# Kernel tuning notes

Hardware: AMD Instinct MI355X
Metric: run time of the kernel (lower is better)

## Reference

```python
import jax, jax.numpy as jnp
import numpy as np


def setup_inputs() -> dict:
    key = jax.random.key(0)
    k1, k2, k3 = jax.random.split(key, 3)
    B, C_in, H, W = 32, 128, 64, 64
    C_out, KH, KW = 256, 3, 3
    x = jax.random.normal(k1, (B, C_in, H, W), dtype=jnp.float32)
    # kaiming_normal fan_out scale ~ sqrt(2 / (C_out*KH*KW)); plain normal is fine for a numeric reference
    weight = jax.random.normal(k2, (C_out, C_in, KH, KW), dtype=jnp.float32) * (2.0 / (C_out * KH * KW)) ** 0.5
    fan_in = C_in * KH * KW
    bound = 1.0 / (fan_in ** 0.5)
    bias = jax.random.uniform(k3, (C_out,), dtype=jnp.float32, minval=-bound, maxval=bound)
    return {"x": x, "weight": weight, "bias": bias}


def reference(x, weight, bias):
    # Equivalent of unfold (im2col) + matmul + fold with stride=1, padding=1:
    # a standard 2D convolution in NCHW/OIHW layout.
    out = jax.lax.conv_general_dilated(
        x, weight,
        window_strides=(1, 1),
        padding=((1, 1), (1, 1)),
        dimension_numbers=("NCHW", "OIHW", "NCHW"),
    )
    return out + bias[None, :, None, None]
```

## Files before the change

### kernel.cpp

```cpp
#include <hip/hip_runtime.h>

typedef __attribute__((ext_vector_type(4))) int   v4i;
typedef __attribute__((ext_vector_type(8))) short s8;
typedef __attribute__((ext_vector_type(4))) float f32x4;
typedef __attribute__((ext_vector_type(16))) float f32x16;

#define GLB __attribute__((address_space(1)))
#define LDS_AS __attribute__((address_space(3)))

__device__ __forceinline__ unsigned short f2bf(float f) {
  unsigned u = __builtin_bit_cast(unsigned, f);
  return (unsigned short)((u + 0x7fffu + ((u >> 16) & 1u)) >> 16);
}

__global__ void wprep(const float* __restrict__ w, unsigned short* __restrict__ ww) {
  int o = blockIdx.x * 256 + threadIdx.x;
  int tap = o >> 15;
  int c   = (o >> 13) & 3;
  int cog = (o >> 10) & 7;
  int kk  = (o >> 9) & 1;
  int lh  = (o >> 8) & 1;
  int l31 = (o >> 3) & 31;
  int e   = o & 7;
  int co = cog * 32 + l31;
  int ci = c * 32 + kk * 16 + lh * 8 + e;
  ww[o] = f2bf(w[(co * 128 + ci) * 9 + tap]);
}

__global__ void xprep(const float* __restrict__ x, unsigned int* __restrict__ xw) {
  __shared__ float tile[128][65];
  int bid = blockIdx.x;
  int b = bid >> 6, h = bid & 63;
  int t = threadIdx.x;
  {
    int wcol = t & 63, cl = t >> 6;
    const float* src = x + ((size_t)(b * 128) * 64 + h) * 64 + wcol;
#pragma unroll
    for (int j = 0; j < 32; ++j) {
      int ci = j * 4 + cl;
      tile[ci][wcol] = src[(size_t)ci * 4096];
    }
  }
  unsigned int* dst = xw + (size_t)((b * 66 + h + 1) * 66) * 64;
  if (t < 128) {
    int col = (t >> 6) ? 65 : 0;
    dst[(size_t)col * 64 + (t & 63)] = 0u;
  }
  if (h == 0 || h == 63) {
    unsigned int* rb = xw + (size_t)(b * 66 + (h == 0 ? 0 : 65)) * 66 * 64;
    for (int j = t; j < 66 * 64; j += 256) rb[j] = 0u;
  }
  __syncthreads();
  {
    int ci2 = (t & 63) * 2, wl = t >> 6;
#pragma unroll
    for (int j = 0; j < 16; ++j) {
      int wcol = j * 4 + wl;
      unsigned p = (unsigned)f2bf(tile[ci2][wcol]) |
                   ((unsigned)f2bf(tile[ci2 + 1][wcol]) << 16);
      dst[(size_t)(wcol + 1) * 64 + (t & 63)] = p;
    }
  }
}

__global__ __launch_bounds__(256, 3) void conv_mfma(
    const unsigned short* __restrict__ xw, const unsigned short* __restrict__ ww,
    const float* __restrict__ bias, float* __restrict__ out) {
  __shared__ unsigned short Xl[204 * 128];
  const int tid = threadIdx.x;
  const int lane = tid & 63;
  const int l31 = lane & 31, lh = lane >> 5;
  const int mw = tid >> 6;
  int bid = blockIdx.x;
  bid = (bid & 7) * 256 + (bid >> 3);
  const int b = bid >> 6, h0 = bid & 63;

  {
    const char* xbase = (const char*)xw;
#pragma unroll
    for (int it = 0; it < 13; ++it) {
      int s = tid + it * 256;
      if (s < 3264) {
        int q = s >> 4, p = s & 15;
        int u = p ^ (q & 15);
        int rr = q / 68, cc = q - rr * 68;
        if (cc > 65) cc = 65;
        unsigned src = (unsigned)((b * 66 + h0 + rr) * 66 + cc) * 256u + (unsigned)u * 16u;
        __builtin_amdgcn_global_load_lds((const GLB unsigned int*)(xbase + src),
                                         (LDS_AS unsigned int*)&Xl[s * 8], 16, 0, 0);
      }
    }
  }

  f32x16 acc[2][2];
#pragma unroll
  for (int m = 0; m < 2; ++m)
#pragma unroll
    for (int n = 0; n < 2; ++n)
#pragma unroll
      for (int e = 0; e < 16; ++e) acc[m][n][e] = 0.f;

  v4i areg[3][4];
  const unsigned abyte = (unsigned)(mw * 4096 + lane * 16);

  #define ALOAD_ASM(slot, step)                                               \
    do {                                                                      \
      unsigned _wo = (unsigned)(step) * 16384u + abyte;                       \
      asm volatile("global_load_dwordx4 %0, %1, %2 offset:0"                  \
                   : "=v"(areg[slot][0]) : "v"(_wo), "s"(ww));                \
      asm volatile("global_load_dwordx4 %0, %1, %2 offset:1024"               \
                   : "=v"(areg[slot][1]) : "v"(_wo), "s"(ww));                \
      asm volatile("global_load_dwordx4 %0, %1, %2 offset:2048"               \
                   : "=v"(areg[slot][2]) : "v"(_wo), "s"(ww));                \
      asm volatile("global_load_dwordx4 %0, %1, %2 offset:3072"               \
                   : "=v"(areg[slot][3]) : "v"(_wo), "s"(ww));                \
    } while (0)

  const char* Xlb = (const char*)Xl;

  __syncthreads();

  ALOAD_ASM(0, 0);
  ALOAD_ASM(1, 1);

#pragma unroll
  for (int s = 0; s < 36; ++s) {
    if (s < 34) ALOAD_ASM((s + 2) % 3, s + 2);

    const int _tap = s >> 2, _c = s & 3;
    const int _kh = _tap / 3, _kw = _tap - _kh * 3;
    const int _qt0 = _kh * 68 + _kw + l31;
    const int _qt1 = _qt0 + 32;
    const int _b0 = _qt0 << 8, _b1 = _qt1 << 8;
    const int _x0 = (_qt0 & 15) ^ lh, _x1 = (_qt1 & 15) ^ lh;
    s8 b00 = *(const s8*)(Xlb + _b0 + (((_c * 4) ^ _x0) << 4));
    s8 b10 = *(const s8*)(Xlb + _b1 + (((_c * 4) ^ _x1) << 4));
    s8 b01 = *(const s8*)(Xlb + _b0 + (((_c * 4 + 2) ^ _x0) << 4));
    s8 b11 = *(const s8*)(Xlb + _b1 + (((_c * 4 + 2) ^ _x1) << 4));

    if (s < 34)      asm volatile("s_waitcnt vmcnt(8)" ::: "memory");
    else if (s == 34) asm volatile("s_waitcnt vmcnt(4)" ::: "memory");
    else              asm volatile("s_waitcnt vmcnt(0)" ::: "memory");
    __builtin_amdgcn_sched_barrier(0);

    const int cs = s % 3;
    __builtin_amdgcn_s_setprio(1);
    acc[0][0] = __builtin_amdgcn_mfma_f32_32x32x16_bf16(__builtin_bit_cast(s8, areg[cs][0]), b00, acc[0][0], 0, 0, 0);
    acc[1][0] = __builtin_amdgcn_mfma_f32_32x32x16_bf16(__builtin_bit_cast(s8, areg[cs][2]), b00, acc[1][0], 0, 0, 0);
    acc[0][1] = __builtin_amdgcn_mfma_f32_32x32x16_bf16(__builtin_bit_cast(s8, areg[cs][0]), b10, acc[0][1], 0, 0, 0);
    acc[1][1] = __builtin_amdgcn_mfma_f32_32x32x16_bf16(__builtin_bit_cast(s8, areg[cs][2]), b10, acc[1][1], 0, 0, 0);
    acc[0][0] = __builtin_amdgcn_mfma_f32_32x32x16_bf16(__builtin_bit_cast(s8, areg[cs][1]), b01, acc[0][0], 0, 0, 0);
    acc[1][0] = __builtin_amdgcn_mfma_f32_32x32x16_bf16(__builtin_bit_cast(s8, areg[cs][3]), b01, acc[1][0], 0, 0, 0);
    acc[0][1] = __builtin_amdgcn_mfma_f32_32x32x16_bf16(__builtin_bit_cast(s8, areg[cs][1]), b11, acc[0][1], 0, 0, 0);
    acc[1][1] = __builtin_amdgcn_mfma_f32_32x32x16_bf16(__builtin_bit_cast(s8, areg[cs][3]), b11, acc[1][1], 0, 0, 0);
    __builtin_amdgcn_s_setprio(0);
  }

#pragma unroll
  for (int m = 0; m < 2; ++m)
#pragma unroll
    for (int rq = 0; rq < 4; ++rq) {
      const int cob = mw * 64 + m * 32 + 8 * rq + 4 * lh;
      const f32x4 bi = *(const f32x4*)(bias + cob);
#pragma unroll
      for (int n = 0; n < 2; ++n) {
        const int wc = n * 32 + l31;
        size_t base = ((size_t)(b * 256 + cob) * 64 + h0) * 64 + wc;
#pragma unroll
        for (int e = 0; e < 4; ++e)
          out[base + (size_t)e * 4096] = acc[m][n][rq * 4 + e] + bi[e];
      }
    }
}

__global__ void conv_naive(const float* __restrict__ x, const float* __restrict__ w,
                           const float* __restrict__ bias, float* __restrict__ out) {
  int i = blockIdx.x * 256 + threadIdx.x;
  int wc = i & 63, h = (i >> 6) & 63, co = (i >> 12) & 255, b = i >> 20;
  float s = bias[co];
  for (int ci = 0; ci < 128; ++ci)
#pragma unroll
    for (int kh = 0; kh < 3; ++kh) {
      int hh = h + kh - 1;
      if ((unsigned)hh >= 64u) continue;
#pragma unroll
      for (int kw = 0; kw < 3; ++kw) {
        int wg = wc + kw - 1;
        if ((unsigned)wg >= 64u) continue;
        s += x[((b * 128 + ci) * 64 + hh) * 64 + wg] *
             w[((co * 128 + ci) * 3 + kh) * 3 + kw];
      }
    }
  out[i] = s;
}

extern "C" void kernel_launch(void* const* d_in, const int* in_sizes, int n_in,
                              void* d_out, int out_size, void* d_ws, size_t ws_size,
                              hipStream_t stream) {
  const float* x    = (const float*)d_in[0];
  const float* w    = (const float*)d_in[1];
  const float* bias = (const float*)d_in[2];
  float* out = (float*)d_out;

  const size_t X_OFF  = 1ull << 20;
  const size_t XBYTES = 32ull * 66 * 66 * 128 * 2;
  const size_t NEED   = X_OFF + XBYTES;

  if (ws_size >= NEED) {
    unsigned short* ww = (unsigned short*)d_ws;
    unsigned short* xq = (unsigned short*)((char*)d_ws + X_OFF);
    hipLaunchKernelGGL(wprep, dim3(1152), dim3(256), 0, stream, w, ww);
    hipLaunchKernelGGL(xprep, dim3(2048), dim3(256), 0, stream, x, (unsigned int*)xq);
    hipLaunchKernelGGL(conv_mfma, dim3(2048), dim3(256), 0, stream, xq, ww, bias, out);
  } else {
    hipLaunchKernelGGL(conv_naive, dim3(131072), dim3(256), 0, stream, x, w, bias, out);
  }
}
```

Before: 108.0 us.

## Halve conv LDS tile by staging channel halves; merge prep kernels

The conv kernel now stages the input tile into LDS in two channel halves (64 channels each). This halves shared memory per block, aiming for higher occupancy, and reorders the K loop so each half's taps are consumed before the next stage. It adds an extra barrier and global-to-LDS stage partway through, and the second stage cannot overlap with compute. The weight and input prep kernels are merged into one launch to save a kernel launch.

```diff
diff --git a/kernel.cpp b/kernel.cpp
--- a/kernel.cpp
+++ b/kernel.cpp
@@ -13,25 +13,26 @@
   return (unsigned short)((u + 0x7fffu + ((u >> 16) & 1u)) >> 16);
 }
 
-__global__ void wprep(const float* __restrict__ w, unsigned short* __restrict__ ww) {
-  int o = blockIdx.x * 256 + threadIdx.x;
-  int tap = o >> 15;
-  int c   = (o >> 13) & 3;
-  int cog = (o >> 10) & 7;
-  int kk  = (o >> 9) & 1;
-  int lh  = (o >> 8) & 1;
-  int l31 = (o >> 3) & 31;
-  int e   = o & 7;
-  int co = cog * 32 + l31;
-  int ci = c * 32 + kk * 16 + lh * 8 + e;
-  ww[o] = f2bf(w[(co * 128 + ci) * 9 + tap]);
-}
-
-__global__ void xprep(const float* __restrict__ x, unsigned int* __restrict__ xw) {
+__global__ void prep(const float* __restrict__ x, const float* __restrict__ w,
+                     unsigned int* __restrict__ xw, unsigned short* __restrict__ ww) {
+  int t = threadIdx.x;
+  if (blockIdx.x >= 2048) {
+    int o = (blockIdx.x - 2048) * 256 + t;
+    int tap = o >> 15;
+    int c   = (o >> 13) & 3;
+    int cog = (o >> 10) & 7;
+    int kk  = (o >> 9) & 1;
+    int lh  = (o >> 8) & 1;
+    int l31 = (o >> 3) & 31;
+    int e   = o & 7;
+    int co = cog * 32 + l31;
+    int ci = c * 32 + kk * 16 + lh * 8 + e;
+    ww[o] = f2bf(w[(co * 128 + ci) * 9 + tap]);
+    return;
+  }
   __shared__ float tile[128][65];
   int bid = blockIdx.x;
   int b = bid >> 6, h = bid & 63;
-  int t = threadIdx.x;
   {
     int wcol = t & 63, cl = t >> 6;
     const float* src = x + ((size_t)(b * 128) * 64 + h) * 64 + wcol;
@@ -66,7 +67,7 @@
 __global__ __launch_bounds__(256, 3) void conv_mfma(
     const unsigned short* __restrict__ xw, const unsigned short* __restrict__ ww,
     const float* __restrict__ bias, float* __restrict__ out) {
-  __shared__ unsigned short Xl[204 * 128];
+  __shared__ unsigned short Xl[204 * 64];
   const int tid = threadIdx.x;
   const int lane = tid & 63;
   const int l31 = lane & 31, lh = lane >> 5;
@@ -75,22 +76,24 @@
   bid = (bid & 7) * 256 + (bid >> 3);
   const int b = bid >> 6, h0 = bid & 63;
 
-  {
-    const char* xbase = (const char*)xw;
-#pragma unroll
-    for (int it = 0; it < 13; ++it) {
-      int s = tid + it * 256;
-      if (s < 3264) {
-        int q = s >> 4, p = s & 15;
-        int u = p ^ (q & 15);
-        int rr = q / 68, cc = q - rr * 68;
-        if (cc > 65) cc = 65;
-        unsigned src = (unsigned)((b * 66 + h0 + rr) * 66 + cc) * 256u + (unsigned)u * 16u;
-        __builtin_amdgcn_global_load_lds((const GLB unsigned int*)(xbase + src),
-                                         (LDS_AS unsigned int*)&Xl[s * 8], 16, 0, 0);
-      }
-    }
-  }
+  #define STAGE(half)                                                          \
+    do {                                                                       \
+      const char* xbase = (const char*)xw + (half) * 128;                      \
+      _Pragma("unroll")                                                        \
+      for (int it = 0; it < 7; ++it) {                                         \
+        int s = tid + it * 256;                                                \
+        if (s < 1632) {                                                        \
+          int q = s >> 3, p = s & 7;                                           \
+          int u = p ^ (q & 7);                                                 \
+          int rr = q / 68, cc = q - rr * 68;                                   \
+          if (cc > 65) cc = 65;                       \
+          unsigned src = (unsigned)((b * 66 + h0 + rr) * 66 + cc) * 256u +     \
+                         (unsigned)u * 16u;                                    \
+          __builtin_amdgcn_global_load_lds((const GLB unsigned int*)(xbase + src), \
+                                           (LDS_AS unsigned int*)&Xl[s * 8], 16, 0, 0); \
+        }                                                                      \
+      }                                                                        \
+    } while (0)
 
   f32x16 acc[2][2];
 #pragma unroll
@@ -103,9 +106,11 @@
   v4i areg[3][4];
   const unsigned abyte = (unsigned)(mw * 4096 + lane * 16);
 
-  #define ALOAD_ASM(slot, step)                                               \
+  #define LSTEP(s) (((((s) % 18) >> 1) * 4) + (((s) / 18) * 2) + ((s) & 1))
+
+  #define ALOAD_ASM(slot, sidx)                                               \
     do {                                                                      \
-      unsigned _wo = (unsigned)(step) * 16384u + abyte;                       \
+      unsigned _wo = (unsigned)(sidx) * 16384u + abyte;                       \
       asm volatile("global_load_dwordx4 %0, %1, %2 offset:0"                  \
                    : "=v"(areg[slot][0]) : "v"(_wo), "s"(ww));                \
       asm volatile("global_load_dwordx4 %0, %1, %2 offset:1024"               \
@@ -118,43 +123,55 @@
 
   const char* Xlb = (const char*)Xl;
 
-  __syncthreads();
-
-  ALOAD_ASM(0, 0);
-  ALOAD_ASM(1, 1);
-
-#pragma unroll
-  for (int s = 0; s < 36; ++s) {
-    if (s < 34) ALOAD_ASM((s + 2) % 3, s + 2);
-
-    const int _tap = s >> 2, _c = s & 3;
-    const int _kh = _tap / 3, _kw = _tap - _kh * 3;
-    const int _qt0 = _kh * 68 + _kw + l31;
-    const int _qt1 = _qt0 + 32;
-    const int _b0 = _qt0 << 8, _b1 = _qt1 << 8;
-    const int _x0 = (_qt0 & 15) ^ lh, _x1 = (_qt1 & 15) ^ lh;
-    s8 b00 = *(const s8*)(Xlb + _b0 + (((_c * 4) ^ _x0) << 4));
-    s8 b10 = *(const s8*)(Xlb + _b1 + (((_c * 4) ^ _x1) << 4));
-    s8 b01 = *(const s8*)(Xlb + _b0 + (((_c * 4 + 2) ^ _x0) << 4));
-    s8 b11 = *(const s8*)(Xlb + _b1 + (((_c * 4 + 2) ^ _x1) << 4));
-
-    if (s < 34)      asm volatile("s_waitcnt vmcnt(8)" ::: "memory");
-    else if (s == 34) asm volatile("s_waitcnt vmcnt(4)" ::: "memory");
-    else              asm volatile("s_waitcnt vmcnt(0)" ::: "memory");
-    __builtin_amdgcn_sched_barrier(0);
-
-    const int cs = s % 3;
-    __builtin_amdgcn_s_setprio(1);
-    acc[0][0] = __builtin_amdgcn_mfma_f32_32x32x16_bf16(__builtin_bit_cast(s8, areg[cs][0]), b00, acc[0][0], 0, 0, 0);
-    acc[1][0] = __builtin_amdgcn_mfma_f32_32x32x16_bf16(__builtin_bit_cast(s8, areg[cs][2]), b00, acc[1][0], 0, 0, 0);
-    acc[0][1] = __builtin_amdgcn_mfma_f32_32x32x16_bf16(__builtin_bit_cast(s8, areg[cs][0]), b10, acc[0][1], 0, 0, 0);
-    acc[1][1] = __builtin_amdgcn_mfma_f32_32x32x16_bf16(__builtin_bit_cast(s8, areg[cs][2]), b10, acc[1][1], 0, 0, 0);
-    acc[0][0] = __builtin_amdgcn_mfma_f32_32x32x16_bf16(__builtin_bit_cast(s8, areg[cs][1]), b01, acc[0][0], 0, 0, 0);
-    acc[1][0] = __builtin_amdgcn_mfma_f32_32x32x16_bf16(__builtin_bit_cast(s8, areg[cs][3]), b01, acc[1][0], 0, 0, 0);
-    acc[0][1] = __builtin_amdgcn_mfma_f32_32x32x16_bf16(__builtin_bit_cast(s8, areg[cs][1]), b11, acc[0][1], 0, 0, 0);
-    acc[1][1] = __builtin_amdgcn_mfma_f32_32x32x16_bf16(__builtin_bit_cast(s8, areg[cs][3]), b11, acc[1][1], 0, 0, 0);
-    __builtin_amdgcn_s_setprio(0);
-  }
+  #define KSTEP(S)                                                            \
+    do {                                                                      \
+      const int _s = (S);                                                     \
+      const bool _iss = (_s < 16) || (_s >= 18 && _s < 34);                   \
+      if (_iss) ALOAD_ASM((_s + 2) % 3, LSTEP(_s + 2));                       \
+      const int _tap = (_s % 18) >> 1, _ch = _s & 1;                          \
+      const int _kh = _tap / 3, _kw = _tap - _kh * 3;                         \
+      const int _q0 = _kh * 68 + _kw + l31, _q1 = _q0 + 32;                   \
+      const int _u0 = _ch * 4 + lh;                                 \
+      const int _u1 = _u0 + 2;                                      \
+      s8 b00 = *(const s8*)(Xlb + (_q0 << 7) + ((_u0 ^ (_q0 & 7)) << 4));     \
+      s8 b10 = *(const s8*)(Xlb + (_q1 << 7) + ((_u0 ^ (_q1 & 7)) << 4));     \
+      s8 b01 = *(const s8*)(Xlb + (_q0 << 7) + ((_u1 ^ (_q0 & 7)) << 4));     \
+      s8 b11 = *(const s8*)(Xlb + (_q1 << 7) + ((_u1 ^ (_q1 & 7)) << 4));     \
+      if (_iss)             asm volatile("s_waitcnt vmcnt(8)" ::: "memory");  \
+      else if ((_s & 1) == 0) asm volatile("s_waitcnt vmcnt(4)" ::: "memory");\
+      else                  asm volatile("s_waitcnt vmcnt(0)" ::: "memory");  \
+      __builtin_amdgcn_sched_barrier(0);                                      \
+      const int _cs = _s % 3;                                                 \
+      __builtin_amdgcn_s_setprio(1);                                          \
+      acc[0][0] = __builtin_amdgcn_mfma_f32_32x32x16_bf16(__builtin_bit_cast(s8, areg[_cs][0]), b00, acc[0][0], 0, 0, 0); \
+      acc[1][0] = __builtin_amdgcn_mfma_f32_32x32x16_bf16(__builtin_bit_cast(s8, areg[_cs][2]), b00, acc[1][0], 0, 0, 0); \
+      acc[0][1] = __builtin_amdgcn_mfma_f32_32x32x16_bf16(__builtin_bit_cast(s8, areg[_cs][0]), b10, acc[0][1], 0, 0, 0); \
+      acc[1][1] = __builtin_amdgcn_mfma_f32_32x32x16_bf16(__builtin_bit_cast(s8, areg[_cs][2]), b10, acc[1][1], 0, 0, 0); \
+      acc[0][0] = __builtin_amdgcn_mfma_f32_32x32x16_bf16(__builtin_bit_cast(s8, areg[_cs][1]), b01, acc[0][0], 0, 0, 0); \
+      acc[1][0] = __builtin_amdgcn_mfma_f32_32x32x16_bf16(__builtin_bit_cast(s8, areg[_cs][3]), b01, acc[1][0], 0, 0, 0); \
+      acc[0][1] = __builtin_amdgcn_mfma_f32_32x32x16_bf16(__builtin_bit_cast(s8, areg[_cs][1]), b11, acc[0][1], 0, 0, 0); \
+      acc[1][1] = __builtin_amdgcn_mfma_f32_32x32x16_bf16(__builtin_bit_cast(s8, areg[_cs][3]), b11, acc[1][1], 0, 0, 0); \
+      __builtin_amdgcn_s_setprio(0);                                          \
+    } while (0)
+
+  STAGE(0);
+  ALOAD_ASM(0, LSTEP(0));
+  ALOAD_ASM(1, LSTEP(1));
+  asm volatile("s_waitcnt vmcnt(8)" ::: "memory");
+  __builtin_amdgcn_sched_barrier(0);
+  __builtin_amdgcn_s_barrier();
+#pragma unroll
+  for (int s = 0; s < 18; ++s) KSTEP(s);
+
+  __builtin_amdgcn_s_barrier();
+  STAGE(1);
+  ALOAD_ASM(0, LSTEP(18));
+  ALOAD_ASM(1, LSTEP(19));
+  asm volatile("s_waitcnt vmcnt(8)" ::: "memory");
+  __builtin_amdgcn_sched_barrier(0);
+  __builtin_amdgcn_s_barrier();
+#pragma unroll
+  for (int s = 18; s < 36; ++s) KSTEP(s);
 
 #pragma unroll
   for (int m = 0; m < 2; ++m)
@@ -209,8 +226,8 @@
   if (ws_size >= NEED) {
     unsigned short* ww = (unsigned short*)d_ws;
     unsigned short* xq = (unsigned short*)((char*)d_ws + X_OFF);
-    hipLaunchKernelGGL(wprep, dim3(1152), dim3(256), 0, stream, w, ww);
-    hipLaunchKernelGGL(xprep, dim3(2048), dim3(256), 0, stream, x, (unsigned int*)xq);
+    hipLaunchKernelGGL(prep, dim3(3200), dim3(256), 0, stream, x, w,
+                       (unsigned int*)xq, ww);
     hipLaunchKernelGGL(conv_mfma, dim3(2048), dim3(256), 0, stream, xq, ww, bias, out);
   } else {
     hipLaunchKernelGGL(conv_naive, dim3(131072), dim3(256), 0, stream, x, w, bias, out);
```

Result: slower. 125.3 us (+15.9%).

## Double-buffer LDS operand reads with inline-asm ds_read and merge prep kernels

Applied to the files above, without the earlier changes.

The conv main loop now reads the input operands from LDS one k-step ahead into a two-slot register buffer. It issues them with inline ds_read_b128 and uses combined vmcnt/lgkmcnt waits, so LDS latency overlaps the MFMA chain. The initial __syncthreads becomes an explicit vmcnt wait plus s_barrier. The two prep kernels (weight repack and input transpose/pad) are fused into one launch split by block index, saving one kernel launch. The explicit waitcnt bookkeeping adds fragility, and the extra operand registers raise register pressure.

```diff
diff --git a/kernel.cpp b/kernel.cpp
--- a/kernel.cpp
+++ b/kernel.cpp
@@ -13,25 +13,26 @@
   return (unsigned short)((u + 0x7fffu + ((u >> 16) & 1u)) >> 16);
 }
 
-__global__ void wprep(const float* __restrict__ w, unsigned short* __restrict__ ww) {
-  int o = blockIdx.x * 256 + threadIdx.x;
-  int tap = o >> 15;
-  int c   = (o >> 13) & 3;
-  int cog = (o >> 10) & 7;
-  int kk  = (o >> 9) & 1;
-  int lh  = (o >> 8) & 1;
-  int l31 = (o >> 3) & 31;
-  int e   = o & 7;
-  int co = cog * 32 + l31;
-  int ci = c * 32 + kk * 16 + lh * 8 + e;
-  ww[o] = f2bf(w[(co * 128 + ci) * 9 + tap]);
-}
-
-__global__ void xprep(const float* __restrict__ x, unsigned int* __restrict__ xw) {
+__global__ void prep(const float* __restrict__ x, const float* __restrict__ w,
+                     unsigned int* __restrict__ xw, unsigned short* __restrict__ ww) {
+  int t = threadIdx.x;
+  if (blockIdx.x >= 2048) {
+    int o = (blockIdx.x - 2048) * 256 + t;
+    int tap = o >> 15;
+    int c   = (o >> 13) & 3;
+    int cog = (o >> 10) & 7;
+    int kk  = (o >> 9) & 1;
+    int lh  = (o >> 8) & 1;
+    int l31 = (o >> 3) & 31;
+    int e   = o & 7;
+    int co = cog * 32 + l31;
+    int ci = c * 32 + kk * 16 + lh * 8 + e;
+    ww[o] = f2bf(w[(co * 128 + ci) * 9 + tap]);
+    return;
+  }
   __shared__ float tile[128][65];
   int bid = blockIdx.x;
   int b = bid >> 6, h = bid & 63;
-  int t = threadIdx.x;
   {
     int wcol = t & 63, cl = t >> 6;
     const float* src = x + ((size_t)(b * 128) * 64 + h) * 64 + wcol;
@@ -74,6 +75,7 @@
   int bid = blockIdx.x;
   bid = (bid & 7) * 256 + (bid >> 3);
   const int b = bid >> 6, h0 = bid & 63;
+  const unsigned xlb = (unsigned)(unsigned long long)((LDS_AS void*)Xl);
 
   {
     const char* xbase = (const char*)xw;
@@ -101,6 +103,7 @@
       for (int e = 0; e < 16; ++e) acc[m][n][e] = 0.f;
 
   v4i areg[3][4];
+  v4i breg[2][4];
   const unsigned abyte = (unsigned)(mw * 4096 + lane * 16);
 
   #define ALOAD_ASM(slot, step)                                               \
@@ -116,45 +119,56 @@
                    : "=v"(areg[slot][3]) : "v"(_wo), "s"(ww));                \
     } while (0)
 
-  const char* Xlb = (const char*)Xl;
-
-  __syncthreads();
+  #define BLOAD_ASM(slot, S)                                                  \
+    do {                                                                      \
+      const int _t = (S) >> 2, _c = (S) & 3;                                  \
+      const int _kh = _t / 3, _kw = _t - _kh * 3;                             \
+      const int _q0 = _kh * 68 + _kw + l31, _q1 = _q0 + 32;                   \
+      const int _xq = (_q0 & 15) ^ lh;             \
+      unsigned _a00 = xlb + (unsigned)((_q0 << 8) + (((_c * 4) ^ _xq) << 4)); \
+      unsigned _a10 = xlb + (unsigned)((_q1 << 8) + (((_c * 4) ^ _xq) << 4)); \
+      unsigned _a01 = xlb + (unsigned)((_q0 << 8) + (((_c * 4 + 2) ^ _xq) << 4)); \
+      unsigned _a11 = xlb + (unsigned)((_q1 << 8) + (((_c * 4 + 2) ^ _xq) << 4)); \
+      asm volatile("ds_read_b128 %0, %1" : "=v"(breg[slot][0]) : "v"(_a00));  \
+      asm volatile("ds_read_b128 %0, %1" : "=v"(breg[slot][1]) : "v"(_a10));  \
+      asm volatile("ds_read_b128 %0, %1" : "=v"(breg[slot][2]) : "v"(_a01));  \
+      asm volatile("ds_read_b128 %0, %1" : "=v"(breg[slot][3]) : "v"(_a11));  \
+    } while (0)
+
+  #define KSTEP(S)                                                            \
+    do {                                                                      \
+      const int _s = (S);                                                     \
+      if (_s < 34) ALOAD_ASM((_s + 2) % 3, _s + 2);                           \
+      if (_s < 35) BLOAD_ASM((_s + 1) & 1, _s + 1);                           \
+      if (_s < 34)                                                            \
+        asm volatile("s_waitcnt vmcnt(8) lgkmcnt(4)" ::: "memory");           \
+      else if (_s == 34)                                                      \
+        asm volatile("s_waitcnt vmcnt(4) lgkmcnt(4)" ::: "memory");           \
+      else                                                                    \
+        asm volatile("s_waitcnt vmcnt(0) lgkmcnt(0)" ::: "memory");           \
+      __builtin_amdgcn_sched_barrier(0);                                      \
+      const int _cs = _s % 3, _bs = _s & 1;                                   \
+      __builtin_amdgcn_s_setprio(1);                                          \
+      acc[0][0] = __builtin_amdgcn_mfma_f32_32x32x16_bf16(__builtin_bit_cast(s8, areg[_cs][0]), __builtin_bit_cast(s8, breg[_bs][0]), acc[0][0], 0, 0, 0); \
+      acc[1][0] = __builtin_amdgcn_mfma_f32_32x32x16_bf16(__builtin_bit_cast(s8, areg[_cs][2]), __builtin_bit_cast(s8, breg[_bs][0]), acc[1][0], 0, 0, 0); \
+      acc[0][1] = __builtin_amdgcn_mfma_f32_32x32x16_bf16(__builtin_bit_cast(s8, areg[_cs][0]), __builtin_bit_cast(s8, breg[_bs][1]), acc[0][1], 0, 0, 0); \
+      acc[1][1] = __builtin_amdgcn_mfma_f32_32x32x16_bf16(__builtin_bit_cast(s8, areg[_cs][2]), __builtin_bit_cast(s8, breg[_bs][1]), acc[1][1], 0, 0, 0); \
+      acc[0][0] = __builtin_amdgcn_mfma_f32_32x32x16_bf16(__builtin_bit_cast(s8, areg[_cs][1]), __builtin_bit_cast(s8, breg[_bs][2]), acc[0][0], 0, 0, 0); \
+      acc[1][0] = __builtin_amdgcn_mfma_f32_32x32x16_bf16(__builtin_bit_cast(s8, areg[_cs][3]), __builtin_bit_cast(s8, breg[_bs][2]), acc[1][0], 0, 0, 0); \
+      acc[0][1] = __builtin_amdgcn_mfma_f32_32x32x16_bf16(__builtin_bit_cast(s8, areg[_cs][1]), __builtin_bit_cast(s8, breg[_bs][3]), acc[0][1], 0, 0, 0); \
+      acc[1][1] = __builtin_amdgcn_mfma_f32_32x32x16_bf16(__builtin_bit_cast(s8, areg[_cs][3]), __builtin_bit_cast(s8, breg[_bs][3]), acc[1][1], 0, 0, 0); \
+      __builtin_amdgcn_s_setprio(0);                                          \
+    } while (0)
 
   ALOAD_ASM(0, 0);
   ALOAD_ASM(1, 1);
-
-#pragma unroll
-  for (int s = 0; s < 36; ++s) {
-    if (s < 34) ALOAD_ASM((s + 2) % 3, s + 2);
-
-    const int _tap = s >> 2, _c = s & 3;
-    const int _kh = _tap / 3, _kw = _tap - _kh * 3;
-    const int _qt0 = _kh * 68 + _kw + l31;
-    const int _qt1 = _qt0 + 32;
-    const int _b0 = _qt0 << 8, _b1 = _qt1 << 8;
-    const int _x0 = (_qt0 & 15) ^ lh, _x1 = (_qt1 & 15) ^ lh;
-    s8 b00 = *(const s8*)(Xlb + _b0 + (((_c * 4) ^ _x0) << 4));
-    s8 b10 = *(const s8*)(Xlb + _b1 + (((_c * 4) ^ _x1) << 4));
-    s8 b01 = *(const s8*)(Xlb + _b0 + (((_c * 4 + 2) ^ _x0) << 4));
-    s8 b11 = *(const s8*)(Xlb + _b1 + (((_c * 4 + 2) ^ _x1) << 4));
-
-    if (s < 34)      asm volatile("s_waitcnt vmcnt(8)" ::: "memory");
-    else if (s == 34) asm volatile("s_waitcnt vmcnt(4)" ::: "memory");
-    else              asm volatile("s_waitcnt vmcnt(0)" ::: "memory");
-    __builtin_amdgcn_sched_barrier(0);
-
-    const int cs = s % 3;
-    __builtin_amdgcn_s_setprio(1);
-    acc[0][0] = __builtin_amdgcn_mfma_f32_32x32x16_bf16(__builtin_bit_cast(s8, areg[cs][0]), b00, acc[0][0], 0, 0, 0);
-    acc[1][0] = __builtin_amdgcn_mfma_f32_32x32x16_bf16(__builtin_bit_cast(s8, areg[cs][2]), b00, acc[1][0], 0, 0, 0);
-    acc[0][1] = __builtin_amdgcn_mfma_f32_32x32x16_bf16(__builtin_bit_cast(s8, areg[cs][0]), b10, acc[0][1], 0, 0, 0);
-    acc[1][1] = __builtin_amdgcn_mfma_f32_32x32x16_bf16(__builtin_bit_cast(s8, areg[cs][2]), b10, acc[1][1], 0, 0, 0);
-    acc[0][0] = __builtin_amdgcn_mfma_f32_32x32x16_bf16(__builtin_bit_cast(s8, areg[cs][1]), b01, acc[0][0], 0, 0, 0);
-    acc[1][0] = __builtin_amdgcn_mfma_f32_32x32x16_bf16(__builtin_bit_cast(s8, areg[cs][3]), b01, acc[1][0], 0, 0, 0);
-    acc[0][1] = __builtin_amdgcn_mfma_f32_32x32x16_bf16(__builtin_bit_cast(s8, areg[cs][1]), b11, acc[0][1], 0, 0, 0);
-    acc[1][1] = __builtin_amdgcn_mfma_f32_32x32x16_bf16(__builtin_bit_cast(s8, areg[cs][3]), b11, acc[1][1], 0, 0, 0);
-    __builtin_amdgcn_s_setprio(0);
-  }
+  asm volatile("s_waitcnt vmcnt(8)" ::: "memory");
+  __builtin_amdgcn_sched_barrier(0);
+  __builtin_amdgcn_s_barrier();
+  BLOAD_ASM(0, 0);
+
+#pragma unroll
+  for (int s = 0; s < 36; ++s) KSTEP(s);
 
 #pragma unroll
   for (int m = 0; m < 2; ++m)
@@ -209,8 +223,8 @@
   if (ws_size >= NEED) {
     unsigned short* ww = (unsigned short*)d_ws;
     unsigned short* xq = (unsigned short*)((char*)d_ws + X_OFF);
-    hipLaunchKernelGGL(wprep, dim3(1152), dim3(256), 0, stream, w, ww);
-    hipLaunchKernelGGL(xprep, dim3(2048), dim3(256), 0, stream, x, (unsigned int*)xq);
+    hipLaunchKernelGGL(prep, dim3(3200), dim3(256), 0, stream, x, w,
+                       (unsigned int*)xq, ww);
     hipLaunchKernelGGL(conv_mfma, dim3(2048), dim3(256), 0, stream, xq, ww, bias, out);
   } else {
     hipLaunchKernelGGL(conv_naive, dim3(131072), dim3(256), 0, stream, x, w, bias, out);
```

Result: faster. 103.2 us (-4.5%).
